# Performance work log

Hardware: AMD Instinct MI355X
Metric: run time of the kernel (lower is better)

Reference implementation:

```python
import jax, jax.numpy as jnp
import numpy as np

B, S, K, N = 4, 2048, 4096, 4096
GS = 128
G = K // GS  # 32 groups


def setup_inputs() -> dict:
    key = jax.random.key(0)
    k1, k2, k3, k4, k5 = jax.random.split(key, 5)
    x = jax.random.normal(k1, (B, S, K), dtype=jnp.float16)
    # packed 4-bit weights: 8 nibbles per int32 along K
    qweight = jax.random.randint(k2, (K // 8, N), 0, 2**31 - 1, dtype=jnp.int32)
    # packed 4-bit zeros: 8 nibbles per int32 along N
    qzeros = jax.random.randint(k3, (G, N // 8), 0, 2**31 - 1, dtype=jnp.int32)
    scales = (jax.random.uniform(k4, (G, N), dtype=jnp.float32) * 0.009 + 0.001).astype(jnp.float16)
    g_idx = (jnp.arange(K, dtype=jnp.int32) // GS).astype(jnp.int32)
    bias = (jax.random.normal(k5, (N,), dtype=jnp.float32) * 0.01).astype(jnp.float16)
    return {"x": x, "qweight": qweight, "qzeros": qzeros, "scales": scales,
            "g_idx": g_idx, "bias": bias}


def _dequantize(qweight, qzeros, scales, g_idx):
    """GPTQ/ExLlama int4 grouped dequant -> fp16 weight [K, N]."""
    shifts = jnp.arange(8, dtype=jnp.int32) * 4
    # unpack qweight along K: [K/8, N] -> [K/8, 8, N] -> [K, N]
    q = ((qweight[:, None, :] >> shifts[None, :, None]) & 0xF).reshape(-1, qweight.shape[1])
    # unpack qzeros along N: [G, N/8] -> [G, N/8, 8] -> [G, N]; GPTQ stores z-1
    z = (((qzeros[:, :, None] >> shifts[None, None, :]) & 0xF).reshape(qzeros.shape[0], -1) + 1)
    zr = z[g_idx]          # [K, N] via per-row group gather (act-order general form)
    sr = scales[g_idx]     # [K, N]
    return (q.astype(sr.dtype) - zr.astype(sr.dtype)) * sr


def reference(x, qweight, qzeros, scales, g_idx, bias):
    W = _dequantize(qweight, qzeros, scales, g_idx)  # [K, N] fp16
    xf = x.reshape(-1, x.shape[-1])                  # [B*S, K]
    out = jnp.matmul(xf, W, preferred_element_type=jnp.float32).astype(x.dtype)
    out = out.reshape(x.shape[:-1] + (W.shape[1],)) + bias
    return out
```

## Files before the change

kernel.cpp:

```cpp
#include <hip/hip_runtime.h>

typedef __attribute__((ext_vector_type(8))) _Float16 halfx8;
typedef __attribute__((ext_vector_type(8))) short short8;
typedef __attribute__((ext_vector_type(4))) float f32x4;

#define DI __device__ __forceinline__

DI unsigned short h2us(_Float16 h) { return __builtin_bit_cast(unsigned short, h); }

DI void gload_lds16(const void* g, void* l) {
  __builtin_amdgcn_global_load_lds(
      (const __attribute__((address_space(1))) void*)g,
      (__attribute__((address_space(3))) void*)l, 16, 0, 0);
}

__global__ void __launch_bounds__(256) conv_x(const float* __restrict__ x,
                                              unsigned short* __restrict__ Xh,
                                              long total) {
  long i = ((long)blockIdx.x * 256 + threadIdx.x) * 8;
  if (i >= total) return;
  f32x4 a = *(const f32x4*)&x[i];
  f32x4 b = *(const f32x4*)&x[i + 4];
  short8 v;
#pragma unroll
  for (int j = 0; j < 4; ++j) {
    v[j] = (short)h2us((_Float16)a[j]);
    v[4 + j] = (short)h2us((_Float16)b[j]);
  }
  *(short8*)&Xh[i] = v;
}

__global__ void __launch_bounds__(256) dequant_wt(
    const int* __restrict__ qweight, const int* __restrict__ qzeros,
    const float* __restrict__ scales, const int* __restrict__ g_idx,
    unsigned short* __restrict__ Wt, int N, int K) {
  int T = blockIdx.x * 256 + threadIdx.x;
  int oct = T & 7;
  int rest = T >> 3;
  int n = rest % N;
  int kblk = rest / N;
  int k = kblk * 64 + oct * 8;
  if (k >= K) return;
  int g = g_idx[k];
  float s = scales[(size_t)g * N + n];
  unsigned zw = (unsigned)qzeros[(size_t)g * (N >> 3) + (n >> 3)];
  int z1 = (int)((zw >> ((n & 7) * 4)) & 0xFu) + 1;
  unsigned qw = (unsigned)qweight[(size_t)(kblk * 8 + oct) * N + n];
  short8 v;
#pragma unroll
  for (int j = 0; j < 8; ++j) {
    int qi = (int)((qw >> (4 * j)) & 0xFu);
    v[j] = (short)h2us((_Float16)((float)(qi - z1) * s));
  }
  *(short8*)&Wt[(size_t)n * K + k] = v;
}

__global__ void __launch_bounds__(512, 2) gemm256(
    const unsigned short* __restrict__ Xh,
    const unsigned short* __restrict__ Wt,
    const float* __restrict__ bias, float* __restrict__ out,
    int M, int N, int K) {
  extern __shared__ unsigned short smem[];
  unsigned short* As = smem;
  unsigned short* Bs = smem + 4 * 8192;

  const int tid = threadIdx.x;
  const int lane = tid & 63;
  const int wave = tid >> 6;
  const int wm = wave >> 2, wn = wave & 3;

  const int cpx = gridDim.x >> 3;
  const int wg = ((int)blockIdx.x & 7) * cpx + ((int)blockIdx.x >> 3);
  const int nbm = M >> 8;
  const int bm = wg % nbm, bn = wg / nbm;
  const int m0 = bm << 8, n0 = bn << 8;

  const int NT = K >> 5;

  const int L0 = tid, L1 = 512 + tid;
  const int r0s = L0 >> 2, c0 = (L0 & 3) ^ ((r0s >> 1) & 3);
  const int r1s = L1 >> 2, c1 = (L1 & 3) ^ ((r1s >> 1) & 3);
  const size_t aoff0 = (size_t)(m0 + r0s) * K + c0 * 8;
  const size_t aoff1 = (size_t)(m0 + r1s) * K + c1 * 8;
  const size_t boff0 = (size_t)(n0 + r0s) * K + c0 * 8;
  const size_t boff1 = (size_t)(n0 + r1s) * K + c1 * 8;

#define STAGE(t)                                               \
  {                                                            \
    int b_ = (t) & 3;                                          \
    int kk_ = (t) << 5;                                        \
    gload_lds16(Xh + aoff0 + kk_, &As[b_ * 8192 + L0 * 8]);    \
    gload_lds16(Xh + aoff1 + kk_, &As[b_ * 8192 + L1 * 8]);    \
    gload_lds16(Wt + boff0 + kk_, &Bs[b_ * 8192 + L0 * 8]);    \
    gload_lds16(Wt + boff1 + kk_, &Bs[b_ * 8192 + L1 * 8]);    \
  }

  STAGE(0); STAGE(1); STAGE(2);
  asm volatile("s_waitcnt vmcnt(8)" ::: "memory");
  __builtin_amdgcn_s_barrier();
  __builtin_amdgcn_sched_barrier(0);

  f32x4 acc[8][4] = {};
  const int lr = lane & 15;
  const int xch = (((lane >> 4) ^ ((lane >> 1) & 3)) * 8);
  const int arow = wm * 128 + lr;
  const int brow = wn * 64 + lr;

  for (int t = 0; t < NT; ++t) {
    if (t + 3 < NT) STAGE(t + 3);

    const unsigned short* Ab = &As[(t & 3) * 8192];
    const unsigned short* Bb = &Bs[(t & 3) * 8192];
    halfx8 af[8], bf[4];
#pragma unroll
    for (int mi = 0; mi < 8; ++mi)
      af[mi] = __builtin_bit_cast(
          halfx8, *(const short8*)&Ab[(arow + mi * 16) * 32 + xch]);
#pragma unroll
    for (int nj = 0; nj < 4; ++nj)
      bf[nj] = __builtin_bit_cast(
          halfx8, *(const short8*)&Bb[(brow + nj * 16) * 32 + xch]);

    __builtin_amdgcn_s_setprio(1);
#pragma unroll
    for (int mi = 0; mi < 8; ++mi)
#pragma unroll
      for (int nj = 0; nj < 4; ++nj)
        acc[mi][nj] = __builtin_amdgcn_mfma_f32_16x16x32_f16(
            af[mi], bf[nj], acc[mi][nj], 0, 0, 0);
    __builtin_amdgcn_s_setprio(0);

    if (t < NT - 3)
      asm volatile("s_waitcnt vmcnt(8)" ::: "memory");
    else if (t == NT - 3)
      asm volatile("s_waitcnt vmcnt(4)" ::: "memory");
    else
      asm volatile("s_waitcnt vmcnt(0)" ::: "memory");
    asm volatile("s_waitcnt lgkmcnt(0)" ::: "memory");
    __builtin_amdgcn_sched_barrier(0);
    __builtin_amdgcn_s_barrier();
    __builtin_amdgcn_sched_barrier(0);
  }
#undef STAGE

#pragma unroll
  for (int nj = 0; nj < 4; ++nj) {
    int col = n0 + wn * 64 + nj * 16 + lr;
    float bv = bias[col];
#pragma unroll
    for (int mi = 0; mi < 8; ++mi) {
      int row0 = m0 + wm * 128 + mi * 16 + ((lane >> 4) << 2);
#pragma unroll
      for (int j = 0; j < 4; ++j)
        out[(size_t)(row0 + j) * N + col] = acc[mi][nj][j] + bv;
    }
  }
}

extern "C" void kernel_launch(void* const* d_in, const int* in_sizes, int n_in,
                              void* d_out, int out_size, void* d_ws,
                              size_t ws_size, hipStream_t stream) {
  const float* x = (const float*)d_in[0];
  const int* qweight = (const int*)d_in[1];
  const int* qzeros = (const int*)d_in[2];
  const float* scales = (const float*)d_in[3];
  const int* g_idx = (const int*)d_in[4];
  const float* bias = (const float*)d_in[5];
  float* out = (float*)d_out;

  const int K = in_sizes[4];
  const int N = in_sizes[5];
  const int M = in_sizes[0] / K;

  unsigned short* Xh = (unsigned short*)d_ws;
  unsigned short* Wtp = (unsigned short*)((char*)d_ws + (size_t)M * K * 2);

  const long xtotal = (long)M * K;
  conv_x<<<dim3((int)(xtotal / 2048)), dim3(256), 0, stream>>>(x, Xh, xtotal);

  const int dq_blocks = (int)(((size_t)N * (K / 8)) / 256);
  dequant_wt<<<dim3(dq_blocks), dim3(256), 0, stream>>>(qweight, qzeros,
                                                        scales, g_idx, Wtp, N, K);

  const int grid = (M / 256) * (N / 256);
  hipFuncSetAttribute((const void*)gemm256,
                      hipFuncAttributeMaxDynamicSharedMemorySize, 131072);
  gemm256<<<dim3(grid), dim3(512), 131072, stream>>>(Xh, Wtp, bias, out,
                                                     M, N, K);
}
```

Measured before the change: 503.4 us.

## Restructure GEMM main loop into 8-phase ping-pong schedule with 64-wide K tiles

Replaces the 4-stage K=32 pipeline with a double-buffered K=64 tile schedule, splitting each iteration into four MFMA sub-phases interleaved with LDS fragment reads and staggered global-to-LDS prefetches for the B and A tiles. The XOR swizzle is changed to suit 64-element rows. The goal is finer overlap of LDS reads, global loads and MFMA work, with fewer stalls per K step. In exchange it adds many more barriers per iteration and keeps only two buffers of prefetch depth, which could expose memory latency.

```diff
diff --git a/kernel.cpp b/kernel.cpp
--- a/kernel.cpp
+++ b/kernel.cpp
@@ -55,15 +55,12 @@
   *(short8*)&Wt[(size_t)n * K + k] = v;
 }
 
-__global__ void __launch_bounds__(512, 2) gemm256(
+__global__ void __launch_bounds__(512, 2) gemm8p(
     const unsigned short* __restrict__ Xh,
     const unsigned short* __restrict__ Wt,
     const float* __restrict__ bias, float* __restrict__ out,
     int M, int N, int K) {
-  extern __shared__ unsigned short smem[];
-  unsigned short* As = smem;
-  unsigned short* Bs = smem + 4 * 8192;
-
+  extern __shared__ unsigned short lds[];
   const int tid = threadIdx.x;
   const int lane = tid & 63;
   const int wave = tid >> 6;
@@ -75,73 +72,141 @@
   const int bm = wg % nbm, bn = wg / nbm;
   const int m0 = bm << 8, n0 = bn << 8;
 
-  const int NT = K >> 5;
-
-  const int L0 = tid, L1 = 512 + tid;
-  const int r0s = L0 >> 2, c0 = (L0 & 3) ^ ((r0s >> 1) & 3);
-  const int r1s = L1 >> 2, c1 = (L1 & 3) ^ ((r1s >> 1) & 3);
-  const size_t aoff0 = (size_t)(m0 + r0s) * K + c0 * 8;
-  const size_t aoff1 = (size_t)(m0 + r1s) * K + c1 * 8;
-  const size_t boff0 = (size_t)(n0 + r0s) * K + c0 * 8;
-  const size_t boff1 = (size_t)(n0 + r1s) * K + c1 * 8;
-
-#define STAGE(t)                                               \
-  {                                                            \
-    int b_ = (t) & 3;                                          \
-    int kk_ = (t) << 5;                                        \
-    gload_lds16(Xh + aoff0 + kk_, &As[b_ * 8192 + L0 * 8]);    \
-    gload_lds16(Xh + aoff1 + kk_, &As[b_ * 8192 + L1 * 8]);    \
-    gload_lds16(Wt + boff0 + kk_, &Bs[b_ * 8192 + L0 * 8]);    \
-    gload_lds16(Wt + boff1 + kk_, &Bs[b_ * 8192 + L1 * 8]);    \
-  }
-
-  STAGE(0); STAGE(1); STAGE(2);
+  const int KT = K >> 6;
+
+  const int srow = tid >> 3;
+  const int scol = ((tid & 7) ^ (srow & 7)) * 8;
+
+#define STG(P, R0, LB, kt)                                                   \
+  {                                                                          \
+    gload_lds16((P) + (size_t)((R0) + srow) * K + (kt) * 64 + scol,          \
+                &lds[(LB) + tid * 8]);                                       \
+    gload_lds16((P) + (size_t)((R0) + srow + 64) * K + (kt) * 64 + scol,     \
+                &lds[(LB) + (tid + 512) * 8]);                               \
+  }
+#define STG_KB(kt)                                                 \
+  {                                                                \
+    STG(Wt, n0, (((kt)&1) * 32768) + 16384, kt);                   \
+    STG(Wt, n0 + 128, (((kt)&1) * 32768) + 16384 + 8192, kt);      \
+  }
+#define STG_KA(kt)                                         \
+  {                                                        \
+    STG(Xh, m0, (((kt)&1) * 32768), kt);                   \
+    STG(Xh, m0 + 128, (((kt)&1) * 32768) + 8192, kt);      \
+  }
+
+  STG_KB(0); STG_KA(0); STG_KB(1); STG_KA(1);
   asm volatile("s_waitcnt vmcnt(8)" ::: "memory");
   __builtin_amdgcn_s_barrier();
   __builtin_amdgcn_sched_barrier(0);
 
   f32x4 acc[8][4] = {};
-  const int lr = lane & 15;
-  const int xch = (((lane >> 4) ^ ((lane >> 1) & 3)) * 8);
-  const int arow = wm * 128 + lr;
-  const int brow = wn * 64 + lr;
-
-  for (int t = 0; t < NT; ++t) {
-    if (t + 3 < NT) STAGE(t + 3);
-
-    const unsigned short* Ab = &As[(t & 3) * 8192];
-    const unsigned short* Bb = &Bs[(t & 3) * 8192];
-    halfx8 af[8], bf[4];
-#pragma unroll
-    for (int mi = 0; mi < 8; ++mi)
-      af[mi] = __builtin_bit_cast(
-          halfx8, *(const short8*)&Ab[(arow + mi * 16) * 32 + xch]);
-#pragma unroll
-    for (int nj = 0; nj < 4; ++nj)
-      bf[nj] = __builtin_bit_cast(
-          halfx8, *(const short8*)&Bb[(brow + nj * 16) * 32 + xch]);
-
-    __builtin_amdgcn_s_setprio(1);
-#pragma unroll
-    for (int mi = 0; mi < 8; ++mi)
-#pragma unroll
-      for (int nj = 0; nj < 4; ++nj)
-        acc[mi][nj] = __builtin_amdgcn_mfma_f32_16x16x32_f16(
-            af[mi], bf[nj], acc[mi][nj], 0, 0, 0);
-    __builtin_amdgcn_s_setprio(0);
-
-    if (t < NT - 3)
+  const int lr = lane & 15, lg = lane >> 4;
+  const int sx0 = (lg ^ (lr & 7)) * 8;
+  const int sx1 = ((4 + lg) ^ (lr & 7)) * 8;
+  const int aB = wm * 8192 + lr * 64;
+  const int bB = 16384 + (wn >> 1) * 8192 + ((wn & 1) * 64 + lr) * 64;
+
+#define RD(ofs) __builtin_bit_cast(halfx8, *(const short8*)&lds[ofs])
+#define LG0                                              \
+  {                                                      \
+    asm volatile("s_waitcnt lgkmcnt(0)" ::: "memory");   \
+    __builtin_amdgcn_sched_barrier(0);                   \
+  }
+#define BAR __builtin_amdgcn_s_barrier()
+
+  for (int kt = 0; kt < KT; ++kt) {
+    const int sE = (kt & 1) * 32768;
+    const bool pf = (kt + 2 < KT);
+    halfx8 af[4][2], bf[4][2];
+
+#pragma unroll
+    for (int mi = 0; mi < 4; ++mi) {
+      af[mi][0] = RD(sE + aB + mi * 1024 + sx0);
+      af[mi][1] = RD(sE + aB + mi * 1024 + sx1);
+    }
+#pragma unroll
+    for (int nj = 0; nj < 2; ++nj) {
+      bf[nj][0] = RD(sE + bB + nj * 1024 + sx0);
+      bf[nj][1] = RD(sE + bB + nj * 1024 + sx1);
+    }
+    BAR; LG0;
+    __builtin_amdgcn_s_setprio(1);
+#pragma unroll
+    for (int mi = 0; mi < 4; ++mi)
+#pragma unroll
+      for (int nj = 0; nj < 2; ++nj)
+#pragma unroll
+        for (int ks = 0; ks < 2; ++ks)
+          acc[mi][nj] = __builtin_amdgcn_mfma_f32_16x16x32_f16(
+              af[mi][ks], bf[nj][ks], acc[mi][nj], 0, 0, 0);
+    __builtin_amdgcn_s_setprio(0);
+    BAR;
+
+#pragma unroll
+    for (int nj = 2; nj < 4; ++nj) {
+      bf[nj][0] = RD(sE + bB + nj * 1024 + sx0);
+      bf[nj][1] = RD(sE + bB + nj * 1024 + sx1);
+    }
+    BAR; LG0;
+    __builtin_amdgcn_s_setprio(1);
+#pragma unroll
+    for (int mi = 0; mi < 4; ++mi)
+#pragma unroll
+      for (int nj = 2; nj < 4; ++nj)
+#pragma unroll
+        for (int ks = 0; ks < 2; ++ks)
+          acc[mi][nj] = __builtin_amdgcn_mfma_f32_16x16x32_f16(
+              af[mi][ks], bf[nj][ks], acc[mi][nj], 0, 0, 0);
+    __builtin_amdgcn_s_setprio(0);
+    BAR;
+    __builtin_amdgcn_sched_barrier(0);
+
+#pragma unroll
+    for (int mi = 0; mi < 4; ++mi) {
+      af[mi][0] = RD(sE + aB + (mi + 4) * 1024 + sx0);
+      af[mi][1] = RD(sE + aB + (mi + 4) * 1024 + sx1);
+    }
+    if (pf) STG_KB(kt + 2);
+    BAR; LG0;
+    __builtin_amdgcn_s_setprio(1);
+#pragma unroll
+    for (int mi = 0; mi < 4; ++mi)
+#pragma unroll
+      for (int nj = 0; nj < 2; ++nj)
+#pragma unroll
+        for (int ks = 0; ks < 2; ++ks)
+          acc[4 + mi][nj] = __builtin_amdgcn_mfma_f32_16x16x32_f16(
+              af[mi][ks], bf[nj][ks], acc[4 + mi][nj], 0, 0, 0);
+    __builtin_amdgcn_s_setprio(0);
+    BAR;
+    __builtin_amdgcn_sched_barrier(0);
+
+    if (pf) STG_KA(kt + 2);
+    BAR;
+    __builtin_amdgcn_s_setprio(1);
+#pragma unroll
+    for (int mi = 0; mi < 4; ++mi)
+#pragma unroll
+      for (int nj = 2; nj < 4; ++nj)
+#pragma unroll
+        for (int ks = 0; ks < 2; ++ks)
+          acc[4 + mi][nj] = __builtin_amdgcn_mfma_f32_16x16x32_f16(
+              af[mi][ks], bf[nj][ks], acc[4 + mi][nj], 0, 0, 0);
+    __builtin_amdgcn_s_setprio(0);
+    if (pf)
       asm volatile("s_waitcnt vmcnt(8)" ::: "memory");
-    else if (t == NT - 3)
-      asm volatile("s_waitcnt vmcnt(4)" ::: "memory");
     else
       asm volatile("s_waitcnt vmcnt(0)" ::: "memory");
-    asm volatile("s_waitcnt lgkmcnt(0)" ::: "memory");
+    BAR;
     __builtin_amdgcn_sched_barrier(0);
-    __builtin_amdgcn_s_barrier();
-    __builtin_amdgcn_sched_barrier(0);
-  }
-#undef STAGE
+  }
+#undef STG
+#undef STG_KA
+#undef STG_KB
+#undef RD
+#undef LG0
+#undef BAR
 
 #pragma unroll
   for (int nj = 0; nj < 4; ++nj) {
@@ -149,7 +214,7 @@
     float bv = bias[col];
 #pragma unroll
     for (int mi = 0; mi < 8; ++mi) {
-      int row0 = m0 + wm * 128 + mi * 16 + ((lane >> 4) << 2);
+      int row0 = m0 + wm * 128 + mi * 16 + (lg << 2);
 #pragma unroll
       for (int j = 0; j < 4; ++j)
         out[(size_t)(row0 + j) * N + col] = acc[mi][nj][j] + bv;
@@ -183,8 +248,8 @@
                                                         scales, g_idx, Wtp, N, K);
 
   const int grid = (M / 256) * (N / 256);
-  hipFuncSetAttribute((const void*)gemm256,
+  hipFuncSetAttribute((const void*)gemm8p,
                       hipFuncAttributeMaxDynamicSharedMemorySize, 131072);
-  gemm256<<<dim3(grid), dim3(512), 131072, stream>>>(Xh, Wtp, bias, out,
-                                                     M, N, K);
-}
+  gemm8p<<<dim3(grid), dim3(512), 131072, stream>>>(Xh, Wtp, bias, out,
+                                                    M, N, K);
+}
```

Result: faster. 488.8 us (-2.9%).
